# Optimization experiments

Hardware: AMD Instinct MI355X
Metric: run time of the kernel (lower is better)

## Reference

```python
import jax, jax.numpy as jnp
import numpy as np

NEG = -1e10  # torch uses -10000000000.0


def setup_inputs() -> dict:
    key = jax.random.key(0)
    ks = jax.random.split(key, 16)
    n, F_, R, D = 8, 64, 36, 1024          # docs, max frames, max ROIs, grounding dim
    MS, W, BH = 16, 10, 768                 # max spans, max span width, bert hidden
    H, ED = 1024, 20                        # mlp hidden, width embed dim
    SD = 2 * BH + BH + ED                   # span embed dim = 2324
    f = lambda k, s: jax.random.normal(k, s, dtype=jnp.float32)
    return dict(
        doc_embeddings=f(ks[0], (n, F_, D)),
        image_embeddings=f(ks[1], (n, R, D)),
        text_mask=jnp.ones((n, F_), jnp.float32),
        image_mask=jnp.ones((n, R), jnp.float32),
        start_end_embeddings=f(ks[2], (n, MS, 2 * BH)),
        continuous_embeddings=f(ks[3], (n, MS, W, BH)),
        width=jax.random.randint(ks[4], (n, MS), 1, W + 1),
        span_mask=jnp.ones((n, MS), jnp.float32),
        attn_w1=f(ks[5], (BH, H)) * 0.02, attn_b1=jnp.zeros((H,), jnp.float32),
        attn_w2=f(ks[6], (H, 1)) * 0.02, attn_b2=jnp.zeros((1,), jnp.float32),
        width_emb=f(ks[7], (5, ED)) * 0.02,
        pw_w1=f(ks[8], (3 * SD, H)) * 0.02, pw_b1=jnp.zeros((H,), jnp.float32),
        pw_w2=f(ks[9], (H, H)) * 0.02, pw_b2=jnp.zeros((H,), jnp.float32),
        pw_w3=f(ks[10], (H, 1)) * 0.02, pw_b3=jnp.zeros((1,), jnp.float32),
    )


def _span_embed(se, cont, width, aw1, ab1, aw2, ab2, wemb):
    # SpanEmbedder: head attention over span tokens + width embedding
    h = jnp.maximum(jnp.einsum('nmtd,dh->nmth', cont, aw1) + ab1, 0.0)
    scores = jnp.einsum('nmth,ho->nmto', h, aw2) + ab2            # (n,ms,W,1)
    tok_mask = jnp.arange(cont.shape[2])[None, None, :] < width[:, :, None]
    scores = jnp.where(tok_mask[..., None], scores, NEG)
    attn = jax.nn.softmax(scores, axis=2)
    weighted = (attn * cont).sum(axis=2)                          # (n,ms,BH)
    wfeat = wemb[jnp.clip(width, 0, 4)]                           # (n,ms,ED)
    return jnp.concatenate([se, weighted, wfeat], axis=-1)


def _grounding_Sg(doc, img, tm, im_):
    # Vectorized over all (s,v) doc pairs; batch-of-1 mean in torch is a no-op.
    att = jnp.einsum('sid,vjd->svij', doc, img)
    mask = tm[:, None, :, None] * im_[None, :, None, :]
    att = att * mask
    att = jnp.where(att != 0.0, att, NEG)
    aw1 = jax.nn.softmax(att * im_[None, :, None, :], axis=-1) * mask
    s1 = (aw1 * att).sum((-1, -2))
    # softmax over transposed axis then permuted back == softmax over frame axis
    aw2 = jax.nn.softmax(att, axis=2) * mask
    s2 = (aw2 * att).sum((-1, -2))
    return s1 + s2  # S_g[s,v] = -loss(s,v)


def _pair_scores(spans, w1, b1, w2, b2, w3, b3):
    # SimplePairWiseClassifier on cat(first, second, first*second), all span pairs
    n, ms, d = spans.shape
    a = spans @ w1[:d]            # contribution of 'first'
    b = spans @ w1[d:2 * d]       # contribution of 'second'
    c = jnp.einsum('sid,vjd,dh->svijh', spans, spans, w1[2 * d:])  # 'first*second'
    h = jnp.maximum(a[:, None, :, None, :] + b[None, :, None, :, :] + c + b1, 0.0)
    h = jnp.maximum(h @ w2 + b2, 0.0)
    return (h @ w3 + b3)[..., 0]  # (n,n,ms,ms)


def _adaptive_Sc(ts, m1):
    # masked version of: text_scores over valid spans; (rowmean.max + colmean.max)/2
    c = m1.sum(-1)  # valid span counts per doc
    rm = (ts * m1[None, :, None, :]).sum(-1) / c[None, :, None]     # (S,V,I)
    max1 = jnp.where(m1[:, None, :] > 0, rm, -jnp.inf).max(-1)      # (S,V)
    cm = (ts * m1[:, None, :, None]).sum(2) / c[:, None, None]      # (S,V,J)
    max2 = jnp.where(m1[None, :, :] > 0, cm, -jnp.inf).max(-1)      # (S,V)
    return (max1 + max2) / 2.0


def reference(doc_embeddings, image_embeddings, text_mask, image_mask,
              start_end_embeddings, continuous_embeddings, width, span_mask,
              attn_w1, attn_b1, attn_w2, attn_b2, width_emb,
              pw_w1, pw_b1, pw_w2, pw_b2, pw_w3, pw_b3):
    n = doc_embeddings.shape[0]
    spans = _span_embed(start_end_embeddings, continuous_embeddings, width,
                        attn_w1, attn_b1, attn_w2, attn_b2, width_emb)
    S_g = _grounding_Sg(doc_embeddings, image_embeddings, text_mask, image_mask)
    ts = _pair_scores(spans, pw_w1, pw_b1, pw_w2, pw_b2, pw_w3, pw_b3)
    S_c = _adaptive_Sc(ts, span_mask)
    mg = jax.nn.softmax(S_g, axis=1)
    mgT = jax.nn.softmax(S_g.T, axis=1)
    mc = jax.nn.softmax(S_c, axis=1)
    loss = -jnp.sum(jnp.log((mg * mc).sum(-1)) + jnp.log((mgT * mc).sum(-1)))
    return loss / n
```

## Files before the change

kernel.cpp:

```cpp
#include <hip/hip_runtime.h>
#include <hip/hip_bf16.h>

#define NEGV -1e10f
#define NEG_INF -3.402823466e38f

typedef __attribute__((ext_vector_type(8))) short short8;
typedef __attribute__((ext_vector_type(4))) float floatx4;

__device__ inline float bf2f(unsigned short u) {
    union { unsigned int i; float f; } c; c.i = ((unsigned int)u) << 16; return c.f;
}
__device__ inline unsigned short f2b(float f) {
    __hip_bfloat16 h = __float2bfloat16(f);
    return *reinterpret_cast<unsigned short*>(&h);
}
__device__ inline unsigned int mul2bf(unsigned int x, unsigned int y) {
    union { unsigned int i; float f; } xl, xh, yl, yh;
    xl.i = x << 16; xh.i = x & 0xffff0000u;
    yl.i = y << 16; yh.i = y & 0xffff0000u;
    unsigned int lo = f2b(xl.f * yl.f);
    unsigned int hi = f2b(xh.f * yh.f);
    return lo | (hi << 16);
}

#define GLL16(g, l) __builtin_amdgcn_global_load_lds( \
    (const __attribute__((address_space(1))) void*)(g), \
    (__attribute__((address_space(3))) void*)(l), 16, 0, 0)

__device__ void transpose_tile(const float* __restrict__ in, int ldin, int krows,
                               unsigned short* __restrict__ out, int ldout,
                               int ktile, int ntile, unsigned short (*L)[66]) {
    int t = threadIdx.x;
    int kt = ktile * 64, nt = ntile * 64;
    int nl = t & 63, g = t >> 6;
#pragma unroll
    for (int i = 0; i < 16; ++i) {
        int kl = g * 16 + i;
        int k = kt + kl;
        float v = (k < krows) ? in[(size_t)k * ldin + nt + nl] : 0.f;
        L[kl][nl] = f2b(v);
    }
    __syncthreads();
    int kl2 = t & 63;
#pragma unroll
    for (int i = 0; i < 16; ++i) {
        int nl2 = g * 16 + i;
        out[(size_t)(nt + nl2) * ldout + kt + kl2] = L[kl2][nl2];
    }
}

__global__ __launch_bounds__(256) void kprep(
    const float* __restrict__ pw_w1, const float* __restrict__ pw_w2,
    const float* __restrict__ aw1, const float* __restrict__ cont,
    unsigned short* __restrict__ w1cT, unsigned short* __restrict__ w1aT,
    unsigned short* __restrict__ w1bT, unsigned short* __restrict__ w2T,
    unsigned short* __restrict__ aw1T, unsigned short* __restrict__ contb,
    float* __restrict__ ts, float* __restrict__ scores, float* __restrict__ attall) {
    __shared__ unsigned short L[64][66];
    int bid = blockIdx.x;
    int tid = threadIdx.x;
    if (bid < 592) {
        transpose_tile(pw_w1 + (size_t)2 * 2324 * 1024, 1024, 2324, w1cT, 2368,
                       bid % 37, bid / 37, L);
    } else if (bid < 1184) {
        int r = bid - 592;
        transpose_tile(pw_w1, 1024, 2324, w1aT, 2368, r % 37, r / 37, L);
    } else if (bid < 1776) {
        int r = bid - 1184;
        transpose_tile(pw_w1 + (size_t)2324 * 1024, 1024, 2324, w1bT, 2368, r % 37, r / 37, L);
    } else if (bid < 2032) {
        int r = bid - 1776;
        transpose_tile(pw_w2, 1024, 1024, w2T, 1024, r % 16, r / 16, L);
    } else if (bid < 2224) {
        int r = bid - 2032;
        transpose_tile(aw1, 1024, 768, aw1T, 768, r % 12, r / 12, L);
    } else if (bid < 6064) {
        int i = (bid - 2224) * 256 + tid;
        contb[i] = f2b(cont[i]);
    } else {
        int i = (bid - 6064) * 256 + tid;
        attall[i] = 0.f;
        if (i < 16384) ts[i] = 0.f;
        if (i < 1280) scores[i] = 0.f;
    }
}

__global__ __launch_bounds__(256) void kscore_gemm(
    const unsigned short* __restrict__ A, const unsigned short* __restrict__ B,
    const float* __restrict__ ab1, const float* __restrict__ aw2,
    float* __restrict__ scores) {
    __shared__ __align__(16) unsigned short Ash[128 * 32];
    __shared__ __align__(16) unsigned short Bsh[128 * 32];
    int tid = threadIdx.x;
    int m0 = blockIdx.y * 128;
    int col0 = blockIdx.x * 128;
    int lane = tid & 63, wave = tid >> 6;
    int wm = wave >> 1, wn = wave & 1;
    int q = lane >> 4, l15 = lane & 15;

    floatx4 acc[4][4];
#pragma unroll
    for (int i = 0; i < 4; ++i)
#pragma unroll
        for (int j = 0; j < 4; ++j) acc[i][j] = (floatx4){0.f, 0.f, 0.f, 0.f};

    int ci0 = wave * 2, ci1 = wave * 2 + 1;
    int p = lane & 3;
    int r0 = ci0 * 16 + (lane >> 2), r1 = ci1 * 16 + (lane >> 2);
    int c0s = p ^ ((r0 >> 1) & 3), c1s = p ^ ((r1 >> 1) & 3);
    const char* gA0 = (const char*)(A + (size_t)(m0 + r0) * 768) + c0s * 16;
    const char* gA1 = (const char*)(A + (size_t)(m0 + r1) * 768) + c1s * 16;
    const char* gB0 = (const char*)(B + (size_t)(col0 + r0) * 768) + c0s * 16;
    const char* gB1 = (const char*)(B + (size_t)(col0 + r1) * 768) + c1s * 16;
    unsigned short* lA0 = Ash + ci0 * 512;
    unsigned short* lA1 = Ash + ci1 * 512;
    unsigned short* lB0 = Bsh + ci0 * 512;
    unsigned short* lB1 = Bsh + ci1 * 512;

    for (int kt = 0; kt < 24; ++kt) {
        __syncthreads();
        GLL16(gA0, lA0);
        GLL16(gA1, lA1);
        GLL16(gB0, lB0);
        GLL16(gB1, lB1);
        gA0 += 64; gA1 += 64; gB0 += 64; gB1 += 64;
        __syncthreads();
        short8 af[4], bfv[4];
#pragma unroll
        for (int i = 0; i < 4; ++i) {
            int rA = wm * 64 + i * 16 + l15;
            af[i] = *(const short8*)(Ash + rA * 32 + (q ^ ((rA >> 1) & 3)) * 8);
        }
#pragma unroll
        for (int j = 0; j < 4; ++j) {
            int rB = wn * 64 + j * 16 + l15;
            bfv[j] = *(const short8*)(Bsh + rB * 32 + (q ^ ((rB >> 1) & 3)) * 8);
        }
#pragma unroll
        for (int i = 0; i < 4; ++i)
#pragma unroll
            for (int j = 0; j < 4; ++j)
                acc[i][j] = __builtin_amdgcn_mfma_f32_16x16x32_bf16(af[i], bfv[j], acc[i][j], 0, 0, 0);
    }

    float b1v[4], w2v[4];
    int nj[4];
#pragma unroll
    for (int j = 0; j < 4; ++j) {
        nj[j] = col0 + wn * 64 + j * 16 + l15;
        b1v[j] = ab1[nj[j]];
        w2v[j] = aw2[nj[j]];
    }
#pragma unroll
    for (int i = 0; i < 4; ++i) {
#pragma unroll
        for (int reg = 0; reg < 4; ++reg) {
            float s = 0.f;
#pragma unroll
            for (int j = 0; j < 4; ++j)
                s += fmaxf(acc[i][j][reg] + b1v[j], 0.f) * w2v[j];
            s += __shfl_down(s, 8, 16);
            s += __shfl_down(s, 4, 16);
            s += __shfl_down(s, 2, 16);
            s += __shfl_down(s, 1, 16);
            if (l15 == 0)
                atomicAdd(&scores[m0 + wm * 64 + i * 16 + q * 4 + reg], s);
        }
    }
}

__global__ __launch_bounds__(256) void k2_assemble(
    const float* __restrict__ se, const float* __restrict__ cont,
    const int* __restrict__ width, const float* __restrict__ scores,
    const float* __restrict__ ab2, const float* __restrict__ wemb,
    unsigned short* __restrict__ sb) {
    int nm = blockIdx.x, tid = threadIdx.x;
    int wd = width[nm];
    float ab2v = ab2[0];
    float sc[10];
    float m = NEG_INF;
#pragma unroll
    for (int t = 0; t < 10; ++t) {
        float s = scores[nm * 10 + t] + ab2v;
        sc[t] = (t < wd) ? s : NEGV;
        m = fmaxf(m, sc[t]);
    }
    float sum = 0.f;
#pragma unroll
    for (int t = 0; t < 10; ++t) { sc[t] = expf(sc[t] - m); sum += sc[t]; }
    float inv = 1.f / sum;
#pragma unroll
    for (int t = 0; t < 10; ++t) sc[t] *= inv;
    const float* cbase = cont + (size_t)nm * 7680;
    unsigned short* srow = sb + (size_t)nm * 2368;
    for (int d = tid; d < 768; d += 256) {
        float acc = 0.f;
#pragma unroll
        for (int t = 0; t < 10; ++t) acc = fmaf(sc[t], cbase[t * 768 + d], acc);
        srow[1536 + d] = f2b(acc);
    }
    for (int idx = tid; idx < 1536; idx += 256) srow[idx] = f2b(se[(size_t)nm * 1536 + idx]);
    if (tid < 20) srow[2304 + tid] = f2b(wemb[min(wd, 4) * 20 + tid]);
    if (tid >= 20 && tid < 64) srow[2304 + tid] = 0;
}

__global__ __launch_bounds__(256) void k3a_att(
    const float* __restrict__ doc, const float* __restrict__ img,
    float* __restrict__ attall) {
    __shared__ float As[32][132];
    __shared__ float Bs[32][100];
    int tid = threadIdx.x;
    int n0 = blockIdx.x * 96;
    int m0 = blockIdx.y * 128;
    int k0base = blockIdx.z * 128;
    int tx = tid & 15, ty = tid >> 4;
    float acc[8][6];
#pragma unroll
    for (int r = 0; r < 8; ++r)
#pragma unroll
        for (int c = 0; c < 6; ++c) acc[r][c] = 0.f;

    for (int kc = 0; kc < 4; ++kc) {
        int k0 = k0base + kc * 32;
        __syncthreads();
#pragma unroll
        for (int p2 = 0; p2 < 4; ++p2) {
            int f = tid + 256 * p2;
            int mm = f >> 3, kq = (f & 7) * 4;
            float4 v = *(const float4*)&doc[(size_t)(m0 + mm) * 1024 + k0 + kq];
            As[kq + 0][mm] = v.x; As[kq + 1][mm] = v.y;
            As[kq + 2][mm] = v.z; As[kq + 3][mm] = v.w;
        }
#pragma unroll
        for (int p2 = 0; p2 < 3; ++p2) {
            int f = tid + 256 * p2;
            int nn = f >> 3, kq = (f & 7) * 4;
            float4 v = *(const float4*)&img[(size_t)(n0 + nn) * 1024 + k0 + kq];
            Bs[kq + 0][nn] = v.x; Bs[kq + 1][nn] = v.y;
            Bs[kq + 2][nn] = v.z; Bs[kq + 3][nn] = v.w;
        }
        __syncthreads();
#pragma unroll 4
        for (int k = 0; k < 32; ++k) {
            float4 a0 = *(const float4*)&As[k][ty * 8];
            float4 a1 = *(const float4*)&As[k][ty * 8 + 4];
            float2 b0 = *(const float2*)&Bs[k][tx * 6];
            float2 b1 = *(const float2*)&Bs[k][tx * 6 + 2];
            float2 b2 = *(const float2*)&Bs[k][tx * 6 + 4];
            float ar[8] = {a0.x, a0.y, a0.z, a0.w, a1.x, a1.y, a1.z, a1.w};
            float br[6] = {b0.x, b0.y, b1.x, b1.y, b2.x, b2.y};
#pragma unroll
            for (int r = 0; r < 8; ++r)
#pragma unroll
                for (int c = 0; c < 6; ++c) acc[r][c] = fmaf(ar[r], br[c], acc[r][c]);
        }
    }
#pragma unroll
    for (int r = 0; r < 8; ++r)
#pragma unroll
        for (int c = 0; c < 6; ++c)
            atomicAdd(&attall[(size_t)(m0 + ty * 8 + r) * 288 + n0 + tx * 6 + c], acc[r][c]);
}

__global__ __launch_bounds__(256) void k3b_reduce(
    const float* __restrict__ attall, const float* __restrict__ tm,
    const float* __restrict__ im, float* __restrict__ Sg) {
    __shared__ float att[64][37];
    __shared__ float tmv[64], imv[36];
    __shared__ float s1sh;
    int b = blockIdx.x;
    int s = b >> 3, v = b & 7;
    int tid = threadIdx.x;
    if (tid < 64) tmv[tid] = tm[s * 64 + tid];
    if (tid >= 64 && tid < 100) imv[tid - 64] = im[v * 36 + (tid - 64)];
    __syncthreads();
    for (int idx = tid; idx < 2304; idx += 256) {
        int i = idx / 36, j = idx - i * 36;
        float raw = attall[(size_t)(s * 64 + i) * 288 + v * 36 + j];
        float x = raw * tmv[i] * imv[j];
        att[i][j] = (x != 0.f) ? x : NEGV;
    }
    __syncthreads();
    float part = 0.f;
    if (tid < 64) {
        int i = tid;
        float mx = NEG_INF;
        for (int j = 0; j < 36; ++j) mx = fmaxf(mx, att[i][j] * imv[j]);
        float sum = 0.f;
        for (int j = 0; j < 36; ++j) sum += expf(att[i][j] * imv[j] - mx);
        float invs = 1.f / sum;
        for (int j = 0; j < 36; ++j) {
            float aw = expf(att[i][j] * imv[j] - mx) * invs * (tmv[i] * imv[j]);
            part += aw * att[i][j];
        }
        for (int off = 32; off > 0; off >>= 1) part += __shfl_down(part, off);
        if (tid == 0) s1sh = part;
    }
    __syncthreads();
    if (tid < 64) {
        float part2 = 0.f;
        if (tid < 36) {
            int j = tid;
            float mx = NEG_INF;
            for (int i = 0; i < 64; ++i) mx = fmaxf(mx, att[i][j]);
            float sum = 0.f;
            for (int i = 0; i < 64; ++i) sum += expf(att[i][j] - mx);
            float invs = 1.f / sum;
            for (int i = 0; i < 64; ++i) {
                float aw = expf(att[i][j] - mx) * invs * (tmv[i] * imv[j]);
                part2 += aw * att[i][j];
            }
        }
        for (int off = 32; off > 0; off >>= 1) part2 += __shfl_down(part2, off);
        if (tid == 0) Sg[s * 8 + v] = s1sh + part2;
    }
}

__global__ __launch_bounds__(256) void k4_gemm(
    const unsigned short* __restrict__ sb, const unsigned short* __restrict__ w1aT,
    const unsigned short* __restrict__ w1bT, float* __restrict__ aout,
    float* __restrict__ bout) {
    __shared__ __align__(16) unsigned short Ash[128 * 32];
    __shared__ __align__(16) unsigned short Bsh[128 * 32];
    int tid = threadIdx.x;
    int col0 = blockIdx.x * 128;
    int half = blockIdx.y;
    const unsigned short* wT = half ? w1bT : w1aT;
    float* outp = half ? bout : aout;
    int lane = tid & 63, wave = tid >> 6;
    int wm = wave >> 1, wn = wave & 1;
    int q = lane >> 4, l15 = lane & 15;

    floatx4 acc[4][4];
#pragma unroll
    for (int i = 0; i < 4; ++i)
#pragma unroll
        for (int j = 0; j < 4; ++j) acc[i][j] = (floatx4){0.f, 0.f, 0.f, 0.f};

    int ci0 = wave * 2, ci1 = wave * 2 + 1;
    int p = lane & 3;
    int r0 = ci0 * 16 + (lane >> 2), r1 = ci1 * 16 + (lane >> 2);
    int c0s = p ^ ((r0 >> 1) & 3), c1s = p ^ ((r1 >> 1) & 3);
    const char* gA0 = (const char*)(sb + (size_t)r0 * 2368) + c0s * 16;
    const char* gA1 = (const char*)(sb + (size_t)r1 * 2368) + c1s * 16;
    const char* gB0 = (const char*)(wT + (size_t)(col0 + r0) * 2368) + c0s * 16;
    const char* gB1 = (const char*)(wT + (size_t)(col0 + r1) * 2368) + c1s * 16;
    unsigned short* lA0 = Ash + ci0 * 512;
    unsigned short* lA1 = Ash + ci1 * 512;
    unsigned short* lB0 = Bsh + ci0 * 512;
    unsigned short* lB1 = Bsh + ci1 * 512;

    for (int kt = 0; kt < 74; ++kt) {
        __syncthreads();
        GLL16(gA0, lA0);
        GLL16(gA1, lA1);
        GLL16(gB0, lB0);
        GLL16(gB1, lB1);
        gA0 += 64; gA1 += 64; gB0 += 64; gB1 += 64;
        __syncthreads();
        short8 af[4], bfv[4];
#pragma unroll
        for (int i = 0; i < 4; ++i) {
            int rA = wm * 64 + i * 16 + l15;
            af[i] = *(const short8*)(Ash + rA * 32 + (q ^ ((rA >> 1) & 3)) * 8);
        }
#pragma unroll
        for (int j = 0; j < 4; ++j) {
            int rB = wn * 64 + j * 16 + l15;
            bfv[j] = *(const short8*)(Bsh + rB * 32 + (q ^ ((rB >> 1) & 3)) * 8);
        }
#pragma unroll
        for (int i = 0; i < 4; ++i)
#pragma unroll
            for (int j = 0; j < 4; ++j)
                acc[i][j] = __builtin_amdgcn_mfma_f32_16x16x32_bf16(af[i], bfv[j], acc[i][j], 0, 0, 0);
    }

    int nj[4];
#pragma unroll
    for (int j = 0; j < 4; ++j) nj[j] = col0 + wn * 64 + j * 16 + l15;
#pragma unroll
    for (int i = 0; i < 4; ++i) {
#pragma unroll
        for (int reg = 0; reg < 4; ++reg) {
            int row = wm * 64 + i * 16 + q * 4 + reg;
#pragma unroll
            for (int j = 0; j < 4; ++j)
                outp[(size_t)row * 1024 + nj[j]] = acc[i][j][reg];
        }
    }
}

__global__ __launch_bounds__(256) void kP2_products(
    const unsigned short* __restrict__ sb, unsigned short* __restrict__ P) {
    int w = blockIdx.x, u = blockIdx.y;
    if (u > w) return;
    int tid = threadIdx.x;
    const uint4* su = (const uint4*)(sb + (size_t)u * 2368);
    const uint4* sw = (const uint4*)(sb + (size_t)w * 2368);
    uint4* out = (uint4*)(P + ((size_t)u * 128 + w) * 2368);
    for (int i = tid; i < 296; i += 256) {
        uint4 a = su[i], b = sw[i];
        uint4 r;
        r.x = mul2bf(a.x, b.x); r.y = mul2bf(a.y, b.y);
        r.z = mul2bf(a.z, b.z); r.w = mul2bf(a.w, b.w);
        out[i] = r;
    }
}

__global__ __launch_bounds__(256) void k5_sym(
    const unsigned short* __restrict__ P, const unsigned short* __restrict__ wT,
    const float* __restrict__ a, const float* __restrict__ b,
    const float* __restrict__ b1, unsigned short* __restrict__ h) {
    __shared__ __align__(16) unsigned short Ash[128 * 32];
    __shared__ __align__(16) unsigned short Bsh[128 * 32];
    int tid = threadIdx.x;
    int bid = blockIdx.x;
    int r8 = bid & 7, t = bid >> 3;
    int c = t & 7, pt = r8 + 8 * (t >> 3);
    const int offs[9] = {0, 16, 30, 42, 52, 60, 66, 70, 72};
    int ut = 0;
#pragma unroll
    for (int k = 1; k < 8; ++k) if (pt >= offs[k]) ut = k;
    int wt = 2 * ut + (pt - offs[ut]);
    int col0 = c * 128;

    int lane = tid & 63, wave = tid >> 6;
    int wm = wave >> 1, wn = wave & 1;
    int q = lane >> 4, l15 = lane & 15;

    floatx4 acc[4][4];
#pragma unroll
    for (int i = 0; i < 4; ++i)
#pragma unroll
        for (int j = 0; j < 4; ++j) acc[i][j] = (floatx4){0.f, 0.f, 0.f, 0.f};

    int ci0 = wave * 2, ci1 = wave * 2 + 1;
    int p = lane & 3;
    int r0 = ci0 * 16 + (lane >> 2), r1 = ci1 * 16 + (lane >> 2);
    int c0s = p ^ ((r0 >> 1) & 3), c1s = p ^ ((r1 >> 1) & 3);
    size_t prow0 = (size_t)(ut * 16 + (r0 >> 3)) * 128 + (wt * 8 + (r0 & 7));
    size_t prow1 = (size_t)(ut * 16 + (r1 >> 3)) * 128 + (wt * 8 + (r1 & 7));
    const char* gA0 = (const char*)(P + prow0 * 2368) + c0s * 16;
    const char* gA1 = (const char*)(P + prow1 * 2368) + c1s * 16;
    const char* gB0 = (const char*)(wT + (size_t)(col0 + r0) * 2368) + c0s * 16;
    const char* gB1 = (const char*)(wT + (size_t)(col0 + r1) * 2368) + c1s * 16;
    unsigned short* lA0 = Ash + ci0 * 512;
    unsigned short* lA1 = Ash + ci1 * 512;
    unsigned short* lB0 = Bsh + ci0 * 512;
    unsigned short* lB1 = Bsh + ci1 * 512;

    for (int kt = 0; kt < 74; ++kt) {
        __syncthreads();
        GLL16(gA0, lA0);
        GLL16(gA1, lA1);
        GLL16(gB0, lB0);
        GLL16(gB1, lB1);
        gA0 += 64; gA1 += 64; gB0 += 64; gB1 += 64;
        __syncthreads();
        short8 af[4], bfv[4];
#pragma unroll
        for (int i = 0; i < 4; ++i) {
            int rA = wm * 64 + i * 16 + l15;
            af[i] = *(const short8*)(Ash + rA * 32 + (q ^ ((rA >> 1) & 3)) * 8);
        }
#pragma unroll
        for (int j = 0; j < 4; ++j) {
            int rB = wn * 64 + j * 16 + l15;
            bfv[j] = *(const short8*)(Bsh + rB * 32 + (q ^ ((rB >> 1) & 3)) * 8);
        }
#pragma unroll
        for (int i = 0; i < 4; ++i)
#pragma unroll
            for (int j = 0; j < 4; ++j)
                acc[i][j] = __builtin_amdgcn_mfma_f32_16x16x32_bf16(af[i], bfv[j], acc[i][j], 0, 0, 0);
    }

    float b1v[4];
    int nj[4];
#pragma unroll
    for (int j = 0; j < 4; ++j) {
        nj[j] = col0 + wn * 64 + j * 16 + l15;
        b1v[j] = b1[nj[j]];
    }
#pragma unroll
    for (int i = 0; i < 4; ++i) {
#pragma unroll
        for (int reg = 0; reg < 4; ++reg) {
            int m = wm * 64 + i * 16 + q * 4 + reg;
            int u = ut * 16 + (m >> 3);
            int w = wt * 8 + (m & 7);
            if (w < u) continue;
            const float* au = a + (size_t)u * 1024;
            const float* bw = b + (size_t)w * 1024;
            unsigned short* hrow = h + ((size_t)u * 128 + w) * 1024;
#pragma unroll
            for (int j = 0; j < 4; ++j)
                hrow[nj[j]] = f2b(fmaxf(acc[i][j][reg] + au[nj[j]] + bw[nj[j]] + b1v[j], 0.f));
            if (w > u) {
                const float* aw_ = a + (size_t)w * 1024;
                const float* bu = b + (size_t)u * 1024;
                unsigned short* hrow2 = h + ((size_t)w * 128 + u) * 1024;
#pragma unroll
                for (int j = 0; j < 4; ++j)
                    hrow2[nj[j]] = f2b(fmaxf(acc[i][j][reg] + aw_[nj[j]] + bu[nj[j]] + b1v[j], 0.f));
            }
        }
    }
}

__global__ __launch_bounds__(256) void k5_mfma(
    const unsigned short* __restrict__ sb, const unsigned short* __restrict__ wT,
    const float* __restrict__ a, const float* __restrict__ b,
    const float* __restrict__ b1, unsigned short* __restrict__ h) {
    __shared__ __align__(16) unsigned short Ash[128 * 32];
    __shared__ __align__(16) unsigned short Bsh[128 * 32];
    int tid = threadIdx.x;
    int u = blockIdx.y;
    int col0 = blockIdx.x * 128;
    int lane = tid & 63, wave = tid >> 6;
    int wm = wave >> 1, wn = wave & 1;
    int q = lane >> 4, l15 = lane & 15;

    floatx4 acc[4][4];
#pragma unroll
    for (int i = 0; i < 4; ++i)
#pragma unroll
        for (int j = 0; j < 4; ++j) acc[i][j] = (floatx4){0.f, 0.f, 0.f, 0.f};

    int r = tid >> 1;
    int cb = (tid & 1) * 2;
    int sw = (r >> 1) & 3;
    const unsigned short* arow = sb + (size_t)r * 2368 + cb * 8;
    const unsigned short* urow = sb + (size_t)u * 2368 + cb * 8;
    const unsigned short* brow = wT + (size_t)(col0 + r) * 2368 + cb * 8;
    unsigned short* awp0 = Ash + r * 32 + (cb ^ sw) * 8;
    unsigned short* awp1 = Ash + r * 32 + ((cb + 1) ^ sw) * 8;
    unsigned short* bwp0 = Bsh + r * 32 + (cb ^ sw) * 8;
    unsigned short* bwp1 = Bsh + r * 32 + ((cb + 1) ^ sw) * 8;

    for (int kt = 0; kt < 74; ++kt) {
        int k0 = kt * 32;
        uint4 av0 = *(const uint4*)(arow + k0);
        uint4 av1 = *(const uint4*)(arow + k0 + 8);
        uint4 uv0 = *(const uint4*)(urow + k0);
        uint4 uv1 = *(const uint4*)(urow + k0 + 8);
        uint4 bv0 = *(const uint4*)(brow + k0);
        uint4 bv1 = *(const uint4*)(brow + k0 + 8);
        __syncthreads();
        uint4 p0, p1;
        p0.x = mul2bf(av0.x, uv0.x); p0.y = mul2bf(av0.y, uv0.y);
        p0.z = mul2bf(av0.z, uv0.z); p0.w = mul2bf(av0.w, uv0.w);
        p1.x = mul2bf(av1.x, uv1.x); p1.y = mul2bf(av1.y, uv1.y);
        p1.z = mul2bf(av1.z, uv1.z); p1.w = mul2bf(av1.w, uv1.w);
        *(uint4*)awp0 = p0;
        *(uint4*)awp1 = p1;
        *(uint4*)bwp0 = bv0;
        *(uint4*)bwp1 = bv1;
        __syncthreads();
// ... 96 lines not shown
        }
#pragma unroll
        for (int i = 0; i < 4; ++i)
#pragma unroll
            for (int j = 0; j < 4; ++j)
                acc[i][j] = __builtin_amdgcn_mfma_f32_16x16x32_bf16(af[i], bfv[j], acc[i][j], 0, 0, 0);
    }

    float b2v[4], w3v[4];
    int nj[4];
#pragma unroll
    for (int j = 0; j < 4; ++j) {
        nj[j] = col0 + wn * 64 + j * 16 + l15;
        b2v[j] = b2[nj[j]];
        w3v[j] = w3[nj[j]];
    }
#pragma unroll
    for (int i = 0; i < 4; ++i) {
#pragma unroll
        for (int reg = 0; reg < 4; ++reg) {
            float s = 0.f;
#pragma unroll
            for (int j = 0; j < 4; ++j)
                s += fmaxf(acc[i][j][reg] + b2v[j], 0.f) * w3v[j];
            s += __shfl_down(s, 8, 16);
            s += __shfl_down(s, 4, 16);
            s += __shfl_down(s, 2, 16);
            s += __shfl_down(s, 1, 16);
            if (l15 == 0)
                atomicAdd(&ts[m0 + wm * 64 + i * 16 + q * 4 + reg], s);
        }
    }
}

__global__ __launch_bounds__(256) void k7_final(
    const float* __restrict__ ts, const float* __restrict__ Sg,
    const float* __restrict__ m1, const float* __restrict__ b3,
    float* __restrict__ out) {
    __shared__ float rmv[1024], cmv[1024];
    __shared__ float cnt[8], m1s[128];
    __shared__ float Sc[64];
    __shared__ float mg[8][8], mgT[8][8], mc[8][8];
    int tid = threadIdx.x;
    if (tid < 128) m1s[tid] = m1[tid];
    __syncthreads();
    if (tid < 8) {
        float c = 0.f;
        for (int k = 0; k < 16; ++k) c += m1s[tid * 16 + k];
        cnt[tid] = c;
    }
    __syncthreads();
    float b3v = b3[0];
    for (int t = tid; t < 1024; t += 256) {
        int s = t >> 7, v = (t >> 4) & 7, x = t & 15;
        const float* row = ts + (size_t)(s * 16 + x) * 128 + v * 16;
        float r = 0.f;
#pragma unroll
        for (int j = 0; j < 16; ++j) r += (row[j] + b3v) * m1s[v * 16 + j];
        rmv[t] = r / cnt[v];
        float c2 = 0.f;
#pragma unroll
        for (int i = 0; i < 16; ++i)
            c2 += (ts[(size_t)(s * 16 + i) * 128 + v * 16 + x] + b3v) * m1s[s * 16 + i];
        cmv[t] = c2 / cnt[s];
    }
    __syncthreads();
    if (tid < 64) {
        int s = tid >> 3, v = tid & 7;
        float max1 = NEG_INF, max2 = NEG_INF;
        for (int i = 0; i < 16; ++i)
            if (m1s[s * 16 + i] > 0.f) max1 = fmaxf(max1, rmv[(s << 7) | (v << 4) | i]);
        for (int j = 0; j < 16; ++j)
            if (m1s[v * 16 + j] > 0.f) max2 = fmaxf(max2, cmv[(s << 7) | (v << 4) | j]);
        Sc[tid] = 0.5f * (max1 + max2);
    }
    __syncthreads();
    if (tid < 8) {
        int r = tid;
        float mx = NEG_INF;
        for (int v = 0; v < 8; ++v) mx = fmaxf(mx, Sg[r * 8 + v]);
        float sm = 0.f;
        for (int v = 0; v < 8; ++v) sm += expf(Sg[r * 8 + v] - mx);
        for (int v = 0; v < 8; ++v) mg[r][v] = expf(Sg[r * 8 + v] - mx) / sm;

        mx = NEG_INF;
        for (int v = 0; v < 8; ++v) mx = fmaxf(mx, Sc[r * 8 + v]);
        sm = 0.f;
        for (int v = 0; v < 8; ++v) sm += expf(Sc[r * 8 + v] - mx);
        for (int v = 0; v < 8; ++v) mc[r][v] = expf(Sc[r * 8 + v] - mx) / sm;

        mx = NEG_INF;
        for (int s2 = 0; s2 < 8; ++s2) mx = fmaxf(mx, Sg[s2 * 8 + r]);
        sm = 0.f;
        for (int s2 = 0; s2 < 8; ++s2) sm += expf(Sg[s2 * 8 + r] - mx);
        for (int s2 = 0; s2 < 8; ++s2) mgT[r][s2] = expf(Sg[s2 * 8 + r] - mx) / sm;
    }
    __syncthreads();
    if (tid == 0) {
        float loss = 0.f;
        for (int r = 0; r < 8; ++r) {
            float d1 = 0.f, d2 = 0.f;
            for (int v = 0; v < 8; ++v) {
                d1 += mg[r][v] * mc[r][v];
                d2 += mgT[r][v] * mc[r][v];
            }
            loss -= logf(d1) + logf(d2);
        }
        out[0] = loss / 8.f;
    }
}

extern "C" void kernel_launch(void* const* d_in, const int* in_sizes, int n_in,
                              void* d_out, int out_size, void* d_ws, size_t ws_size,
                              hipStream_t stream) {
    const float* doc   = (const float*)d_in[0];
    const float* img   = (const float*)d_in[1];
    const float* tm    = (const float*)d_in[2];
    const float* im    = (const float*)d_in[3];
    const float* se    = (const float*)d_in[4];
    const float* cont  = (const float*)d_in[5];
    const int*   width = (const int*)d_in[6];
    const float* m1    = (const float*)d_in[7];
    const float* aw1   = (const float*)d_in[8];
    const float* ab1   = (const float*)d_in[9];
    const float* aw2   = (const float*)d_in[10];
    const float* ab2   = (const float*)d_in[11];
    const float* wemb  = (const float*)d_in[12];
    const float* pw_w1 = (const float*)d_in[13];
    const float* pw_b1 = (const float*)d_in[14];
    const float* pw_w2 = (const float*)d_in[15];
    const float* pw_b2 = (const float*)d_in[16];
    const float* pw_w3 = (const float*)d_in[17];
    const float* pw_b3 = (const float*)d_in[18];
    float* out = (float*)d_out;

    char* ws = (char*)d_ws;
    float* scores           = (float*)(ws + 0);
    float* a                = (float*)(ws + 8192);
    float* b                = (float*)(ws + 532480);
    float* Sg               = (float*)(ws + 1056768);
    float* ts               = (float*)(ws + 1057024);
    unsigned short* sb      = (unsigned short*)(ws + 1122560);
    unsigned short* w1cT    = (unsigned short*)(ws + 1728768);
    unsigned short* w2T     = (unsigned short*)(ws + 6578432);
    unsigned short* h       = (unsigned short*)(ws + 8675584);
    unsigned short* P       = (unsigned short*)(ws + 42230016);
    const size_t NEED_P = 42230016ull + 16384ull * 2368ull * 2ull;
    unsigned short* contb   = (unsigned short*)(ws + 8675584);
    unsigned short* aw1T    = (unsigned short*)(ws + 10641664);
    unsigned short* w1aT    = (unsigned short*)(ws + 12214528);
    unsigned short* w1bT    = (unsigned short*)(ws + 17064192);
    float* attall           = (float*)(ws + 21913856);

    kprep<<<8368, 256, 0, stream>>>(pw_w1, pw_w2, aw1, cont, w1cT, w1aT, w1bT,
                                    w2T, aw1T, contb, ts, scores, attall);
    kscore_gemm<<<dim3(8, 10), 256, 0, stream>>>(contb, aw1T, ab1, aw2, scores);
    k2_assemble<<<128, 256, 0, stream>>>(se, cont, width, scores, ab2, wemb, sb);
    k3a_att<<<dim3(3, 4, 8), 256, 0, stream>>>(doc, img, attall);
    k3b_reduce<<<64, 256, 0, stream>>>(attall, tm, im, Sg);
    k4_gemm<<<dim3(8, 2), 256, 0, stream>>>(sb, w1aT, w1bT, a, b);
    if (ws_size >= NEED_P) {
        kP2_products<<<dim3(128, 128), 256, 0, stream>>>(sb, P);
        k5_sym<<<576, 256, 0, stream>>>(P, w1cT, a, b, pw_b1, h);
    } else {
        k5_mfma<<<dim3(8, 128), 256, 0, stream>>>(sb, w1cT, a, b, pw_b1, h);
    }
    k6_gemm<<<1024, 256, 0, stream>>>(h, w2T, pw_b2, pw_w3, ts);
    k7_final<<<1, 256, 0, stream>>>(ts, Sg, m1, pw_b3, out);
}
```

Before: 402.7 us.

## Fuse independent mid-stage kernels into two launches and split-K the a/b GEMM

New measurement: 337.5 us (median of 2 runs). 1.19x faster.

```diff
diff --git a/kernel.cpp b/kernel.cpp
--- a/kernel.cpp
+++ b/kernel.cpp
@@ -55,7 +55,8 @@
     unsigned short* __restrict__ w1cT, unsigned short* __restrict__ w1aT,
     unsigned short* __restrict__ w1bT, unsigned short* __restrict__ w2T,
     unsigned short* __restrict__ aw1T, unsigned short* __restrict__ contb,
-    float* __restrict__ ts, float* __restrict__ scores, float* __restrict__ attall) {
+    float* __restrict__ ts, float* __restrict__ scores, float* __restrict__ attall,
+    float* __restrict__ a, float* __restrict__ b) {
     __shared__ unsigned short L[64][66];
     int bid = blockIdx.x;
     int tid = threadIdx.x;
@@ -77,95 +78,159 @@
     } else if (bid < 6064) {
         int i = (bid - 2224) * 256 + tid;
         contb[i] = f2b(cont[i]);
-    } else {
+    } else if (bid < 8368) {
         int i = (bid - 6064) * 256 + tid;
         attall[i] = 0.f;
         if (i < 16384) ts[i] = 0.f;
         if (i < 1280) scores[i] = 0.f;
-    }
-}
-
-__global__ __launch_bounds__(256) void kscore_gemm(
-    const unsigned short* __restrict__ A, const unsigned short* __restrict__ B,
+    } else {
+        int i = (bid - 8368) * 256 + tid;
+        a[i] = 0.f;
+        b[i] = 0.f;
+    }
+}
+
+__global__ __launch_bounds__(256) void kmidA(
+    const unsigned short* __restrict__ contb, const unsigned short* __restrict__ aw1T,
     const float* __restrict__ ab1, const float* __restrict__ aw2,
-    float* __restrict__ scores) {
+    float* __restrict__ scores,
+    const float* __restrict__ doc, const float* __restrict__ img,
+    float* __restrict__ attall) {
     __shared__ __align__(16) unsigned short Ash[128 * 32];
     __shared__ __align__(16) unsigned short Bsh[128 * 32];
+    __shared__ float As[32][132];
+    __shared__ float Bs[32][100];
+    int bid = blockIdx.x;
     int tid = threadIdx.x;
-    int m0 = blockIdx.y * 128;
-    int col0 = blockIdx.x * 128;
-    int lane = tid & 63, wave = tid >> 6;
-    int wm = wave >> 1, wn = wave & 1;
-    int q = lane >> 4, l15 = lane & 15;
-
-    floatx4 acc[4][4];
-#pragma unroll
-    for (int i = 0; i < 4; ++i)
-#pragma unroll
-        for (int j = 0; j < 4; ++j) acc[i][j] = (floatx4){0.f, 0.f, 0.f, 0.f};
-
-    int ci0 = wave * 2, ci1 = wave * 2 + 1;
-    int p = lane & 3;
-    int r0 = ci0 * 16 + (lane >> 2), r1 = ci1 * 16 + (lane >> 2);
-    int c0s = p ^ ((r0 >> 1) & 3), c1s = p ^ ((r1 >> 1) & 3);
-    const char* gA0 = (const char*)(A + (size_t)(m0 + r0) * 768) + c0s * 16;
-    const char* gA1 = (const char*)(A + (size_t)(m0 + r1) * 768) + c1s * 16;
-    const char* gB0 = (const char*)(B + (size_t)(col0 + r0) * 768) + c0s * 16;
-    const char* gB1 = (const char*)(B + (size_t)(col0 + r1) * 768) + c1s * 16;
-    unsigned short* lA0 = Ash + ci0 * 512;
-    unsigned short* lA1 = Ash + ci1 * 512;
-    unsigned short* lB0 = Bsh + ci0 * 512;
-    unsigned short* lB1 = Bsh + ci1 * 512;
-
-    for (int kt = 0; kt < 24; ++kt) {
-        __syncthreads();
-        GLL16(gA0, lA0);
-        GLL16(gA1, lA1);
-        GLL16(gB0, lB0);
-        GLL16(gB1, lB1);
-        gA0 += 64; gA1 += 64; gB0 += 64; gB1 += 64;
-        __syncthreads();
-        short8 af[4], bfv[4];
+
+    if (bid < 80) {
+        int m0 = (bid >> 3) * 128;
+        int col0 = (bid & 7) * 128;
+        int lane = tid & 63, wave = tid >> 6;
+        int wm = wave >> 1, wn = wave & 1;
+        int q = lane >> 4, l15 = lane & 15;
+
+        floatx4 acc[4][4];
+#pragma unroll
+        for (int i = 0; i < 4; ++i)
+#pragma unroll
+            for (int j = 0; j < 4; ++j) acc[i][j] = (floatx4){0.f, 0.f, 0.f, 0.f};
+
+        int ci0 = wave * 2, ci1 = wave * 2 + 1;
+        int p = lane & 3;
+        int r0 = ci0 * 16 + (lane >> 2), r1 = ci1 * 16 + (lane >> 2);
+        int c0s = p ^ ((r0 >> 1) & 3), c1s = p ^ ((r1 >> 1) & 3);
+        const char* gA0 = (const char*)(contb + (size_t)(m0 + r0) * 768) + c0s * 16;
+        const char* gA1 = (const char*)(contb + (size_t)(m0 + r1) * 768) + c1s * 16;
+        const char* gB0 = (const char*)(aw1T + (size_t)(col0 + r0) * 768) + c0s * 16;
+        const char* gB1 = (const char*)(aw1T + (size_t)(col0 + r1) * 768) + c1s * 16;
+        unsigned short* lA0 = Ash + ci0 * 512;
+        unsigned short* lA1 = Ash + ci1 * 512;
+        unsigned short* lB0 = Bsh + ci0 * 512;
+        unsigned short* lB1 = Bsh + ci1 * 512;
+
+        for (int kt = 0; kt < 24; ++kt) {
+            __syncthreads();
+            GLL16(gA0, lA0);
+            GLL16(gA1, lA1);
+            GLL16(gB0, lB0);
+            GLL16(gB1, lB1);
+            gA0 += 64; gA1 += 64; gB0 += 64; gB1 += 64;
+            __syncthreads();
+            short8 af[4], bfv[4];
+#pragma unroll
+            for (int i = 0; i < 4; ++i) {
+                int rA = wm * 64 + i * 16 + l15;
+                af[i] = *(const short8*)(Ash + rA * 32 + (q ^ ((rA >> 1) & 3)) * 8);
+            }
+#pragma unroll
+            for (int j = 0; j < 4; ++j) {
+                int rB = wn * 64 + j * 16 + l15;
+                bfv[j] = *(const short8*)(Bsh + rB * 32 + (q ^ ((rB >> 1) & 3)) * 8);
+            }
+#pragma unroll
+            for (int i = 0; i < 4; ++i)
+#pragma unroll
+                for (int j = 0; j < 4; ++j)
+                    acc[i][j] = __builtin_amdgcn_mfma_f32_16x16x32_bf16(af[i], bfv[j], acc[i][j], 0, 0, 0);
+        }
+
+        float b1v[4], w2v[4];
+        int nj[4];
+#pragma unroll
+        for (int j = 0; j < 4; ++j) {
+            nj[j] = col0 + wn * 64 + j * 16 + l15;
+            b1v[j] = ab1[nj[j]];
+            w2v[j] = aw2[nj[j]];
+        }
 #pragma unroll
         for (int i = 0; i < 4; ++i) {
-            int rA = wm * 64 + i * 16 + l15;
-            af[i] = *(const short8*)(Ash + rA * 32 + (q ^ ((rA >> 1) & 3)) * 8);
-        }
-#pragma unroll
-        for (int j = 0; j < 4; ++j) {
-            int rB = wn * 64 + j * 16 + l15;
-            bfv[j] = *(const short8*)(Bsh + rB * 32 + (q ^ ((rB >> 1) & 3)) * 8);
-        }
-#pragma unroll
-        for (int i = 0; i < 4; ++i)
-#pragma unroll
-            for (int j = 0; j < 4; ++j)
-                acc[i][j] = __builtin_amdgcn_mfma_f32_16x16x32_bf16(af[i], bfv[j], acc[i][j], 0, 0, 0);
-    }
-
-    float b1v[4], w2v[4];
-    int nj[4];
-#pragma unroll
-    for (int j = 0; j < 4; ++j) {
-        nj[j] = col0 + wn * 64 + j * 16 + l15;
-        b1v[j] = ab1[nj[j]];
-        w2v[j] = aw2[nj[j]];
-    }
-#pragma unroll
-    for (int i = 0; i < 4; ++i) {
-#pragma unroll
-        for (int reg = 0; reg < 4; ++reg) {
-            float s = 0.f;
-#pragma unroll
-            for (int j = 0; j < 4; ++j)
-                s += fmaxf(acc[i][j][reg] + b1v[j], 0.f) * w2v[j];
-            s += __shfl_down(s, 8, 16);
-            s += __shfl_down(s, 4, 16);
-            s += __shfl_down(s, 2, 16);
-            s += __shfl_down(s, 1, 16);
-            if (l15 == 0)
-                atomicAdd(&scores[m0 + wm * 64 + i * 16 + q * 4 + reg], s);
-        }
+#pragma unroll
+            for (int reg = 0; reg < 4; ++reg) {
+                float s = 0.f;
+#pragma unroll
+                for (int j = 0; j < 4; ++j)
+                    s += fmaxf(acc[i][j][reg] + b1v[j], 0.f) * w2v[j];
+                s += __shfl_down(s, 8, 16);
+                s += __shfl_down(s, 4, 16);
+                s += __shfl_down(s, 2, 16);
+                s += __shfl_down(s, 1, 16);
+                if (l15 == 0)
+                    atomicAdd(&scores[m0 + wm * 64 + i * 16 + q * 4 + reg], s);
+            }
+        }
+    } else {
+        int r = bid - 80;
+        int n0 = (r % 3) * 96;
+        int m0 = ((r / 3) & 3) * 128;
+        int k0base = (r / 12) * 128;
+        int tx = tid & 15, ty = tid >> 4;
+        float acc[8][6];
+#pragma unroll
+        for (int rr = 0; rr < 8; ++rr)
+#pragma unroll
+            for (int c = 0; c < 6; ++c) acc[rr][c] = 0.f;
+
+        for (int kc = 0; kc < 4; ++kc) {
+            int k0 = k0base + kc * 32;
+            __syncthreads();
+#pragma unroll
+            for (int p2 = 0; p2 < 4; ++p2) {
+                int f = tid + 256 * p2;
+                int mm = f >> 3, kq = (f & 7) * 4;
+                float4 v = *(const float4*)&doc[(size_t)(m0 + mm) * 1024 + k0 + kq];
+                As[kq + 0][mm] = v.x; As[kq + 1][mm] = v.y;
+                As[kq + 2][mm] = v.z; As[kq + 3][mm] = v.w;
+            }
+#pragma unroll
+            for (int p2 = 0; p2 < 3; ++p2) {
+                int f = tid + 256 * p2;
+                int nn = f >> 3, kq = (f & 7) * 4;
+                float4 v = *(const float4*)&img[(size_t)(n0 + nn) * 1024 + k0 + kq];
+                Bs[kq + 0][nn] = v.x; Bs[kq + 1][nn] = v.y;
+                Bs[kq + 2][nn] = v.z; Bs[kq + 3][nn] = v.w;
+            }
+            __syncthreads();
+#pragma unroll 4
+            for (int k = 0; k < 32; ++k) {
+                float4 a0 = *(const float4*)&As[k][ty * 8];
+                float4 a1 = *(const float4*)&As[k][ty * 8 + 4];
+                float2 b0 = *(const float2*)&Bs[k][tx * 6];
+                float2 b1 = *(const float2*)&Bs[k][tx * 6 + 2];
+                float2 b2 = *(const float2*)&Bs[k][tx * 6 + 4];
+                float ar[8] = {a0.x, a0.y, a0.z, a0.w, a1.x, a1.y, a1.z, a1.w};
+                float br[6] = {b0.x, b0.y, b1.x, b1.y, b2.x, b2.y};
+#pragma unroll
+                for (int rr = 0; rr < 8; ++rr)
+#pragma unroll
+                    for (int c = 0; c < 6; ++c) acc[rr][c] = fmaf(ar[rr], br[c], acc[rr][c]);
+            }
+        }
+#pragma unroll
+        for (int rr = 0; rr < 8; ++rr)
+#pragma unroll
+            for (int c = 0; c < 6; ++c)
+                atomicAdd(&attall[(size_t)(m0 + ty * 8 + rr) * 288 + n0 + tx * 6 + c], acc[rr][c]);
     }
 }
 
@@ -204,207 +269,150 @@
     if (tid >= 20 && tid < 64) srow[2304 + tid] = 0;
 }
 
-__global__ __launch_bounds__(256) void k3a_att(
-    const float* __restrict__ doc, const float* __restrict__ img,
-    float* __restrict__ attall) {
-    __shared__ float As[32][132];
-    __shared__ float Bs[32][100];
-    int tid = threadIdx.x;
-    int n0 = blockIdx.x * 96;
-    int m0 = blockIdx.y * 128;
-    int k0base = blockIdx.z * 128;
-    int tx = tid & 15, ty = tid >> 4;
-    float acc[8][6];
-#pragma unroll
-    for (int r = 0; r < 8; ++r)
-#pragma unroll
-        for (int c = 0; c < 6; ++c) acc[r][c] = 0.f;
-
-    for (int kc = 0; kc < 4; ++kc) {
-        int k0 = k0base + kc * 32;
-        __syncthreads();
-#pragma unroll
-        for (int p2 = 0; p2 < 4; ++p2) {
-            int f = tid + 256 * p2;
-            int mm = f >> 3, kq = (f & 7) * 4;
-            float4 v = *(const float4*)&doc[(size_t)(m0 + mm) * 1024 + k0 + kq];
-            As[kq + 0][mm] = v.x; As[kq + 1][mm] = v.y;
-            As[kq + 2][mm] = v.z; As[kq + 3][mm] = v.w;
-        }
-#pragma unroll
-        for (int p2 = 0; p2 < 3; ++p2) {
-            int f = tid + 256 * p2;
-            int nn = f >> 3, kq = (f & 7) * 4;
-            float4 v = *(const float4*)&img[(size_t)(n0 + nn) * 1024 + k0 + kq];
-            Bs[kq + 0][nn] = v.x; Bs[kq + 1][nn] = v.y;
-            Bs[kq + 2][nn] = v.z; Bs[kq + 3][nn] = v.w;
-        }
-        __syncthreads();
-#pragma unroll 4
-        for (int k = 0; k < 32; ++k) {
-            float4 a0 = *(const float4*)&As[k][ty * 8];
-            float4 a1 = *(const float4*)&As[k][ty * 8 + 4];
-            float2 b0 = *(const float2*)&Bs[k][tx * 6];
-            float2 b1 = *(const float2*)&Bs[k][tx * 6 + 2];
-            float2 b2 = *(const float2*)&Bs[k][tx * 6 + 4];
-            float ar[8] = {a0.x, a0.y, a0.z, a0.w, a1.x, a1.y, a1.z, a1.w};
-            float br[6] = {b0.x, b0.y, b1.x, b1.y, b2.x, b2.y};
-#pragma unroll
-            for (int r = 0; r < 8; ++r)
-#pragma unroll
-                for (int c = 0; c < 6; ++c) acc[r][c] = fmaf(ar[r], br[c], acc[r][c]);
-        }
-    }
-#pragma unroll
-    for (int r = 0; r < 8; ++r)
-#pragma unroll
-        for (int c = 0; c < 6; ++c)
-            atomicAdd(&attall[(size_t)(m0 + ty * 8 + r) * 288 + n0 + tx * 6 + c], acc[r][c]);
-}
-
-__global__ __launch_bounds__(256) void k3b_reduce(
+__global__ __launch_bounds__(256) void kmidB(
+    const unsigned short* __restrict__ sb, unsigned short* __restrict__ P, int doP,
+    const unsigned short* __restrict__ w1aT, const unsigned short* __restrict__ w1bT,
+    float* __restrict__ aout, float* __restrict__ bout,
     const float* __restrict__ attall, const float* __restrict__ tm,
     const float* __restrict__ im, float* __restrict__ Sg) {
+    __shared__ __align__(16) unsigned short Ash[128 * 32];
+    __shared__ __align__(16) unsigned short Bsh[128 * 32];
     __shared__ float att[64][37];
     __shared__ float tmv[64], imv[36];
     __shared__ float s1sh;
-    int b = blockIdx.x;
-    int s = b >> 3, v = b & 7;
+    int bid = blockIdx.x;
     int tid = threadIdx.x;
-    if (tid < 64) tmv[tid] = tm[s * 64 + tid];
-    if (tid >= 64 && tid < 100) imv[tid - 64] = im[v * 36 + (tid - 64)];
-    __syncthreads();
-    for (int idx = tid; idx < 2304; idx += 256) {
-        int i = idx / 36, j = idx - i * 36;
-        float raw = attall[(size_t)(s * 64 + i) * 288 + v * 36 + j];
-        float x = raw * tmv[i] * imv[j];
-        att[i][j] = (x != 0.f) ? x : NEGV;
-    }
-    __syncthreads();
-    float part = 0.f;
-    if (tid < 64) {
-        int i = tid;
-        float mx = NEG_INF;
-        for (int j = 0; j < 36; ++j) mx = fmaxf(mx, att[i][j] * imv[j]);
-        float sum = 0.f;
-        for (int j = 0; j < 36; ++j) sum += expf(att[i][j] * imv[j] - mx);
-        float invs = 1.f / sum;
-        for (int j = 0; j < 36; ++j) {
-            float aw = expf(att[i][j] * imv[j] - mx) * invs * (tmv[i] * imv[j]);
-            part += aw * att[i][j];
-        }
-        for (int off = 32; off > 0; off >>= 1) part += __shfl_down(part, off);
-        if (tid == 0) s1sh = part;
-    }
-    __syncthreads();
-    if (tid < 64) {
-        float part2 = 0.f;
-        if (tid < 36) {
-            int j = tid;
+
+    if (bid < 16384) {
+        if (!doP) return;
+        int w = bid & 127, u = bid >> 7;
+        if (u > w) return;
+        const uint4* su = (const uint4*)(sb + (size_t)u * 2368);
+        const uint4* sw = (const uint4*)(sb + (size_t)w * 2368);
+        uint4* out = (uint4*)(P + ((size_t)u * 128 + w) * 2368);
+        for (int i = tid; i < 296; i += 256) {
+            uint4 a = su[i], b = sw[i];
+            uint4 r;
+            r.x = mul2bf(a.x, b.x); r.y = mul2bf(a.y, b.y);
+            r.z = mul2bf(a.z, b.z); r.w = mul2bf(a.w, b.w);
+            out[i] = r;
+        }
+    } else if (bid < 16512) {
+        int r = bid - 16384;
+        int col0 = (r & 7) * 128;
+        int half = (r >> 3) & 1;
+        int kz = r >> 4;
+        int kt0 = (74 * kz) / 8, kt1 = (74 * (kz + 1)) / 8;
+        const unsigned short* wT = half ? w1bT : w1aT;
+        float* outp = half ? bout : aout;
+        int lane = tid & 63, wave = tid >> 6;
+        int wm = wave >> 1, wn = wave & 1;
+        int q = lane >> 4, l15 = lane & 15;
+
+        floatx4 acc[4][4];
+#pragma unroll
+        for (int i = 0; i < 4; ++i)
+#pragma unroll
+            for (int j = 0; j < 4; ++j) acc[i][j] = (floatx4){0.f, 0.f, 0.f, 0.f};
+
+        int ci0 = wave * 2, ci1 = wave * 2 + 1;
+        int p = lane & 3;
+        int r0 = ci0 * 16 + (lane >> 2), r1 = ci1 * 16 + (lane >> 2);
+        int c0s = p ^ ((r0 >> 1) & 3), c1s = p ^ ((r1 >> 1) & 3);
+        const char* gA0 = (const char*)(sb + (size_t)r0 * 2368) + c0s * 16 + kt0 * 64;
+        const char* gA1 = (const char*)(sb + (size_t)r1 * 2368) + c1s * 16 + kt0 * 64;
+        const char* gB0 = (const char*)(wT + (size_t)(col0 + r0) * 2368) + c0s * 16 + kt0 * 64;
+        const char* gB1 = (const char*)(wT + (size_t)(col0 + r1) * 2368) + c1s * 16 + kt0 * 64;
+        unsigned short* lA0 = Ash + ci0 * 512;
+        unsigned short* lA1 = Ash + ci1 * 512;
+        unsigned short* lB0 = Bsh + ci0 * 512;
+        unsigned short* lB1 = Bsh + ci1 * 512;
+
+        for (int kt = kt0; kt < kt1; ++kt) {
+            __syncthreads();
+            GLL16(gA0, lA0);
+            GLL16(gA1, lA1);
+            GLL16(gB0, lB0);
+            GLL16(gB1, lB1);
+            gA0 += 64; gA1 += 64; gB0 += 64; gB1 += 64;
+            __syncthreads();
+            short8 af[4], bfv[4];
+#pragma unroll
+            for (int i = 0; i < 4; ++i) {
+                int rA = wm * 64 + i * 16 + l15;
+                af[i] = *(const short8*)(Ash + rA * 32 + (q ^ ((rA >> 1) & 3)) * 8);
+            }
+#pragma unroll
+            for (int j = 0; j < 4; ++j) {
+                int rB = wn * 64 + j * 16 + l15;
+                bfv[j] = *(const short8*)(Bsh + rB * 32 + (q ^ ((rB >> 1) & 3)) * 8);
+            }
+#pragma unroll
+            for (int i = 0; i < 4; ++i)
+#pragma unroll
+                for (int j = 0; j < 4; ++j)
+                    acc[i][j] = __builtin_amdgcn_mfma_f32_16x16x32_bf16(af[i], bfv[j], acc[i][j], 0, 0, 0);
+        }
+
+        int nj[4];
+#pragma unroll
+        for (int j = 0; j < 4; ++j) nj[j] = col0 + wn * 64 + j * 16 + l15;
+#pragma unroll
+        for (int i = 0; i < 4; ++i) {
+#pragma unroll
+            for (int reg = 0; reg < 4; ++reg) {
+                int row = wm * 64 + i * 16 + q * 4 + reg;
+#pragma unroll
+                for (int j = 0; j < 4; ++j)
+                    atomicAdd(&outp[(size_t)row * 1024 + nj[j]], acc[i][j][reg]);
+            }
+        }
+    } else {
+        int r2 = bid - 16512;
+        int s = r2 >> 3, v = r2 & 7;
+        if (tid < 64) tmv[tid] = tm[s * 64 + tid];
+        if (tid >= 64 && tid < 100) imv[tid - 64] = im[v * 36 + (tid - 64)];
+        __syncthreads();
+        for (int idx = tid; idx < 2304; idx += 256) {
+            int i = idx / 36, j = idx - i * 36;
+            float raw = attall[(size_t)(s * 64 + i) * 288 + v * 36 + j];
+            float x = raw * tmv[i] * imv[j];
+            att[i][j] = (x != 0.f) ? x : NEGV;
+        }
+        __syncthreads();
+        float part = 0.f;
+        if (tid < 64) {
+            int i = tid;
             float mx = NEG_INF;
-            for (int i = 0; i < 64; ++i) mx = fmaxf(mx, att[i][j]);
+            for (int j = 0; j < 36; ++j) mx = fmaxf(mx, att[i][j] * imv[j]);
             float sum = 0.f;
-            for (int i = 0; i < 64; ++i) sum += expf(att[i][j] - mx);
+            for (int j = 0; j < 36; ++j) sum += expf(att[i][j] * imv[j] - mx);
             float invs = 1.f / sum;
-            for (int i = 0; i < 64; ++i) {
-                float aw = expf(att[i][j] - mx) * invs * (tmv[i] * imv[j]);
-                part2 += aw * att[i][j];
-            }
-        }
-        for (int off = 32; off > 0; off >>= 1) part2 += __shfl_down(part2, off);
-        if (tid == 0) Sg[s * 8 + v] = s1sh + part2;
-    }
-}
-
-__global__ __launch_bounds__(256) void k4_gemm(
-    const unsigned short* __restrict__ sb, const unsigned short* __restrict__ w1aT,
-    const unsigned short* __restrict__ w1bT, float* __restrict__ aout,
-    float* __restrict__ bout) {
-    __shared__ __align__(16) unsigned short Ash[128 * 32];
-    __shared__ __align__(16) unsigned short Bsh[128 * 32];
-    int tid = threadIdx.x;
-    int col0 = blockIdx.x * 128;
-    int half = blockIdx.y;
-    const unsigned short* wT = half ? w1bT : w1aT;
-    float* outp = half ? bout : aout;
-    int lane = tid & 63, wave = tid >> 6;
-    int wm = wave >> 1, wn = wave & 1;
-    int q = lane >> 4, l15 = lane & 15;
-
-    floatx4 acc[4][4];
-#pragma unroll
-    for (int i = 0; i < 4; ++i)
-#pragma unroll
-        for (int j = 0; j < 4; ++j) acc[i][j] = (floatx4){0.f, 0.f, 0.f, 0.f};
-
-    int ci0 = wave * 2, ci1 = wave * 2 + 1;
-    int p = lane & 3;
-    int r0 = ci0 * 16 + (lane >> 2), r1 = ci1 * 16 + (lane >> 2);
-    int c0s = p ^ ((r0 >> 1) & 3), c1s = p ^ ((r1 >> 1) & 3);
-    const char* gA0 = (const char*)(sb + (size_t)r0 * 2368) + c0s * 16;
-    const char* gA1 = (const char*)(sb + (size_t)r1 * 2368) + c1s * 16;
-    const char* gB0 = (const char*)(wT + (size_t)(col0 + r0) * 2368) + c0s * 16;
-    const char* gB1 = (const char*)(wT + (size_t)(col0 + r1) * 2368) + c1s * 16;
-    unsigned short* lA0 = Ash + ci0 * 512;
-    unsigned short* lA1 = Ash + ci1 * 512;
-    unsigned short* lB0 = Bsh + ci0 * 512;
-    unsigned short* lB1 = Bsh + ci1 * 512;
-
-    for (int kt = 0; kt < 74; ++kt) {
+            for (int j = 0; j < 36; ++j) {
+                float aw = expf(att[i][j] * imv[j] - mx) * invs * (tmv[i] * imv[j]);
+                part += aw * att[i][j];
+            }
+            for (int off = 32; off > 0; off >>= 1) part += __shfl_down(part, off);
+            if (tid == 0) s1sh = part;
+        }
         __syncthreads();
-        GLL16(gA0, lA0);
-        GLL16(gA1, lA1);
-        GLL16(gB0, lB0);
-        GLL16(gB1, lB1);
-        gA0 += 64; gA1 += 64; gB0 += 64; gB1 += 64;
-        __syncthreads();
-        short8 af[4], bfv[4];
-#pragma unroll
-        for (int i = 0; i < 4; ++i) {
-            int rA = wm * 64 + i * 16 + l15;
-            af[i] = *(const short8*)(Ash + rA * 32 + (q ^ ((rA >> 1) & 3)) * 8);
-        }
-#pragma unroll
-        for (int j = 0; j < 4; ++j) {
-            int rB = wn * 64 + j * 16 + l15;
-            bfv[j] = *(const short8*)(Bsh + rB * 32 + (q ^ ((rB >> 1) & 3)) * 8);
-        }
-#pragma unroll
-        for (int i = 0; i < 4; ++i)
-#pragma unroll
-            for (int j = 0; j < 4; ++j)
-                acc[i][j] = __builtin_amdgcn_mfma_f32_16x16x32_bf16(af[i], bfv[j], acc[i][j], 0, 0, 0);
-    }
-
-    int nj[4];
-#pragma unroll
-    for (int j = 0; j < 4; ++j) nj[j] = col0 + wn * 64 + j * 16 + l15;
-#pragma unroll
-    for (int i = 0; i < 4; ++i) {
-#pragma unroll
-        for (int reg = 0; reg < 4; ++reg) {
-            int row = wm * 64 + i * 16 + q * 4 + reg;
-#pragma unroll
-            for (int j = 0; j < 4; ++j)
-                outp[(size_t)row * 1024 + nj[j]] = acc[i][j][reg];
-        }
-    }
-}
-
-__global__ __launch_bounds__(256) void kP2_products(
-    const unsigned short* __restrict__ sb, unsigned short* __restrict__ P) {
-    int w = blockIdx.x, u = blockIdx.y;
-    if (u > w) return;
-    int tid = threadIdx.x;
-    const uint4* su = (const uint4*)(sb + (size_t)u * 2368);
-    const uint4* sw = (const uint4*)(sb + (size_t)w * 2368);
-    uint4* out = (uint4*)(P + ((size_t)u * 128 + w) * 2368);
-    for (int i = tid; i < 296; i += 256) {
-        uint4 a = su[i], b = sw[i];
-        uint4 r;
-        r.x = mul2bf(a.x, b.x); r.y = mul2bf(a.y, b.y);
-        r.z = mul2bf(a.z, b.z); r.w = mul2bf(a.w, b.w);
-        out[i] = r;
+        if (tid < 64) {
+            float part2 = 0.f;
+            if (tid < 36) {
+                int j = tid;
+                float mx = NEG_INF;
+                for (int i = 0; i < 64; ++i) mx = fmaxf(mx, att[i][j]);
+                float sum = 0.f;
+                for (int i = 0; i < 64; ++i) sum += expf(att[i][j] - mx);
+                float invs = 1.f / sum;
+                for (int i = 0; i < 64; ++i) {
+                    float aw = expf(att[i][j] - mx) * invs * (tmv[i] * imv[j]);
+                    part2 += aw * att[i][j];
+                }
+            }
+            for (int off = 32; off > 0; off >>= 1) part2 += __shfl_down(part2, off);
+            if (tid == 0) Sg[s * 8 + v] = s1sh + part2;
+        }
     }
 }
 
@@ -807,15 +815,14 @@
     unsigned short* w1bT    = (unsigned short*)(ws + 17064192);
     float* attall           = (float*)(ws + 21913856);
 
-    kprep<<<8368, 256, 0, stream>>>(pw_w1, pw_w2, aw1, cont, w1cT, w1aT, w1bT,
-                                    w2T, aw1T, contb, ts, scores, attall);
-    kscore_gemm<<<dim3(8, 10), 256, 0, stream>>>(contb, aw1T, ab1, aw2, scores);
+    int doP = (ws_size >= NEED_P) ? 1 : 0;
+
+    kprep<<<8880, 256, 0, stream>>>(pw_w1, pw_w2, aw1, cont, w1cT, w1aT, w1bT,
+                                    w2T, aw1T, contb, ts, scores, attall, a, b);
+    kmidA<<<176, 256, 0, stream>>>(contb, aw1T, ab1, aw2, scores, doc, img, attall);
     k2_assemble<<<128, 256, 0, stream>>>(se, cont, width, scores, ab2, wemb, sb);
-    k3a_att<<<dim3(3, 4, 8), 256, 0, stream>>>(doc, img, attall);
-    k3b_reduce<<<64, 256, 0, stream>>>(attall, tm, im, Sg);
-    k4_gemm<<<dim3(8, 2), 256, 0, stream>>>(sb, w1aT, w1bT, a, b);
-    if (ws_size >= NEED_P) {
-        kP2_products<<<dim3(128, 128), 256, 0, stream>>>(sb, P);
+    kmidB<<<16576, 256, 0, stream>>>(sb, P, doP, w1aT, w1bT, a, b, attall, tm, im, Sg);
+    if (doP) {
         k5_sym<<<576, 256, 0, stream>>>(P, w1cT, a, b, pw_b1, h);
     } else {
         k5_mfma<<<dim3(8, 128), 256, 0, stream>>>(sb, w1cT, a, b, pw_b1, h);
```
